# Kernel optimization log

Measured on AMD Instinct MI355X. Metric: run time of the kernel, lower is better.

Reference implementation:

```python
import jax, jax.numpy as jnp
import numpy as np

B, T, N, F_, H, C, E = 8, 16, 1024, 128, 8, 32, 32768
D = H * C  # 256 = hidden_channels * num_heads
NEG_SLOPE = 0.2


def setup_inputs() -> dict:
    key = jax.random.key(0)
    ks = jax.random.split(key, 16)
    p = lambda k, shape: (jax.random.normal(k, shape, jnp.float32) * 0.05)
    inp = {
        "x": jax.random.normal(ks[0], (B, T, N, F_), jnp.float32),
        "edge_index": jax.random.randint(ks[1], (2, E), 0, N, jnp.int64),
        "edge_weight": jax.random.uniform(ks[2], (E,), jnp.float32),
        # GAT layer 1
        "W1": p(ks[3], (F_, D)), "att_src1": p(ks[4], (H, C)),
        "att_dst1": p(ks[5], (H, C)), "b1": jnp.zeros((D,), jnp.float32),
        # GAT layer 2
        "W2": p(ks[6], (D, D)), "att_src2": p(ks[7], (H, C)),
        "att_dst2": p(ks[8], (H, C)), "b2": jnp.zeros((D,), jnp.float32),
        # LSTM (torch gate order: i, f, g, o)
        "lstm_Wih": p(ks[9], (4 * D, D)), "lstm_Whh": p(ks[10], (4 * D, D)),
        "lstm_bih": jnp.zeros((4 * D,), jnp.float32),
        "lstm_bhh": jnp.zeros((4 * D,), jnp.float32),
        # edge predictors
        "Wp": p(ks[11], (1, D)), "bp": jnp.zeros((1,), jnp.float32),
        "Wc": p(ks[12], (1, D)), "bc": jnp.zeros((1,), jnp.float32),
    }
    return inp


def _gat_layer(x2d, src, dst, W, a_src, a_dst, b):
    # x2d: [N, Fin]; src/dst: [Et] (self-loops already appended)
    h = (x2d @ W).reshape(N, H, C)              # [N, H, C]
    es = jnp.sum(h * a_src, axis=-1)            # [N, H]
    ed = jnp.sum(h * a_dst, axis=-1)            # [N, H]
    e = jax.nn.leaky_relu(es[src] + ed[dst], NEG_SLOPE)  # [Et, H]
    m = jax.ops.segment_max(e, dst, num_segments=N)      # [N, H]
    m = jnp.where(jnp.isfinite(m), m, 0.0)
    pnum = jnp.exp(e - m[dst])                  # [Et, H]
    denom = jax.ops.segment_sum(pnum, dst, num_segments=N)
    alpha = pnum / (denom[dst] + 1e-16)         # segment softmax over incoming edges
    out = jax.ops.segment_sum(alpha[:, :, None] * h[src], dst, num_segments=N)
    return out.reshape(N, D) + b                # concat heads + bias


def _forward(x, edge_index, edge_weight, W1, att_src1, att_dst1, b1,
             W2, att_src2, att_dst2, b2, lstm_Wih, lstm_Whh, lstm_bih,
             lstm_bhh, Wp, bp, Wc, bc):
    # GATConv ignores edge_weight when edge_dim is None (lin_edge is None).
    sl = jnp.arange(N, dtype=edge_index.dtype)
    src = jnp.concatenate([edge_index[0], sl])  # add_self_loops=True
    dst = jnp.concatenate([edge_index[1], sl])

    def per_graph(xi):  # xi: [N, F_]
        hh = jax.nn.relu(_gat_layer(xi, src, dst, W1, att_src1, att_dst1, b1))
        hh = jax.nn.relu(_gat_layer(hh, src, dst, W2, att_src2, att_dst2, b2))
        return hh  # [N, D]

    # stack timesteps then batches == reshape to [B*T, N, F_]
    hall = jax.vmap(per_graph)(x.reshape(B * T, N, F_))  # [B*T, N, D]

    # LSTM over the node dimension (batch_first=True, batch=B*T, seq=N)
    def step(carry, xt):
        hprev, cprev = carry
        z = xt @ lstm_Wih.T + hprev @ lstm_Whh.T + lstm_bih + lstm_bhh
        i, f, g, o = jnp.split(z, 4, axis=-1)
        c = jax.nn.sigmoid(f) * cprev + jax.nn.sigmoid(i) * jnp.tanh(g)
        hcur = jax.nn.sigmoid(o) * jnp.tanh(c)
        return (hcur, hcur * 0 + c)[0:1] * 0 or ((hcur, c), hcur)

    def step2(carry, xt):
        hprev, cprev = carry
        z = xt @ lstm_Wih.T + hprev @ lstm_Whh.T + lstm_bih + lstm_bhh
        i, f, g, o = jnp.split(z, 4, axis=-1)
        c = jax.nn.sigmoid(f) * cprev + jax.nn.sigmoid(i) * jnp.tanh(g)
        hcur = jax.nn.sigmoid(o) * jnp.tanh(c)
        return (hcur, c), hcur

    init = (jnp.zeros((B * T, D), hall.dtype), jnp.zeros((B * T, D), hall.dtype))
    _, hs = jax.lax.scan(step2, init, jnp.swapaxes(hall, 0, 1))  # [N, B*T, D]
    out = jnp.swapaxes(hs, 0, 1)      # [B*T, N, D]

    xsel = out[::T]                   # [B, N, D]
    xflat = xsel.reshape(B * N, D)
    xe = xflat[edge_index[0]] * xflat[edge_index[1]]  # [E, D]
    edge_weights_pred = xe @ Wp.T + bp                # [E, 1]
    logits = (xe @ Wc.T + bc).squeeze(-1)             # [E]
    return edge_weights_pred, logits


def reference(x, edge_index, edge_weight, W1, att_src1, att_dst1, b1,
              W2, att_src2, att_dst2, b2, lstm_Wih, lstm_Whh, lstm_bih,
              lstm_bhh, Wp, bp, Wc, bc):
    return _forward(x, edge_index, edge_weight, W1, att_src1, att_dst1, b1,
                    W2, att_src2, att_dst2, b2, lstm_Wih, lstm_Whh, lstm_bih,
                    lstm_bhh, Wp, bp, Wc, bc)
```

## Files before the change

kernel.cpp:

```cpp
#include <hip/hip_runtime.h>
#include <math.h>

#define NN 1024
#define FF 128
#define DD 256
#define HH 8
#define CC 32
#define EE 32768
#define NEDGE (EE + NN)

typedef unsigned int u32x2 __attribute__((ext_vector_type(2)));

__device__ __forceinline__ float sigf(float x) { return 1.0f / (1.0f + expf(-x)); }
__device__ __forceinline__ float fsig(float x) { return 1.0f / (1.0f + __expf(-x)); }
__device__ __forceinline__ float ftanh(float x) { return 2.0f / (1.0f + __expf(-2.0f * x)) - 1.0f; }

__device__ __forceinline__ void store_l2_u64(unsigned long long* p, unsigned long long v) {
  asm volatile("global_store_dwordx2 %0, %1, off sc0" :: "v"(p), "v"(v) : "memory");
}
__device__ __forceinline__ u32x2 load_l2_u64(const unsigned long long* p) {
  u32x2 r;
  asm volatile("global_load_dwordx2 %0, %1, off sc0\n\ts_waitcnt vmcnt(0)"
               : "=v"(r) : "v"(p) : "memory");
  return r;
}

__device__ __forceinline__ void barrier_lds() {
  asm volatile("s_waitcnt lgkmcnt(0)" ::: "memory");
  __builtin_amdgcn_sched_barrier(0);
  __builtin_amdgcn_s_barrier();
}

__global__ void k_count(const int* __restrict__ ei, int* __restrict__ count) {
  int k = blockIdx.x * blockDim.x + threadIdx.x;
  if (k >= NEDGE) return;
  int d = (k < EE) ? ei[EE + k] : (k - EE);
  atomicAdd(&count[d], 1);
}

__global__ void k_scan(const int* __restrict__ count, int* __restrict__ rowptr, int* __restrict__ cursor) {
  __shared__ int buf[NN];
  int t = threadIdx.x;
  int c = count[t];
  buf[t] = c;
  __syncthreads();
  for (int off = 1; off < NN; off <<= 1) {
    int add = (t >= off) ? buf[t - off] : 0;
    __syncthreads();
    buf[t] += add;
    __syncthreads();
  }
  int inc = buf[t];
  rowptr[t] = inc - c;
  cursor[t] = inc - c;
  if (t == NN - 1) rowptr[NN] = inc;
}

__global__ void k_scatter(const int* __restrict__ ei, int* __restrict__ cursor, int* __restrict__ csrc) {
  int k = blockIdx.x * blockDim.x + threadIdx.x;
  if (k >= NEDGE) return;
  int s, d;
  if (k < EE) { s = ei[k]; d = ei[EE + k]; }
  else        { s = k - EE; d = k - EE; }
  int pos = atomicAdd(&cursor[d], 1);
  csrc[pos] = s;
}

template<bool BT, bool ADDB>
__global__ __launch_bounds__(256) void k_gemm(const float* __restrict__ A, const float* __restrict__ B,
    const float* __restrict__ bias1, const float* __restrict__ bias2, float* __restrict__ C,
    int M, int N, int K) {
  __shared__ float At[64][17];
  __shared__ float Bt[16][65];
  const int tid = threadIdx.x;
  const int m0 = blockIdx.x * 64, n0 = blockIdx.y * 64;
  const int tx = tid & 15, ty = tid >> 4;
  float acc[4][4] = {{0.f, 0.f, 0.f, 0.f}};
  for (int k0 = 0; k0 < K; k0 += 16) {
    {
      int rr = tid >> 2, kl = (tid & 3) * 4;
      float4 a = *(const float4*)(A + (m0 + rr) * K + k0 + kl);
      At[rr][kl] = a.x; At[rr][kl + 1] = a.y; At[rr][kl + 2] = a.z; At[rr][kl + 3] = a.w;
    }
    if (BT) {
      int nn = tid >> 2, kl = (tid & 3) * 4;
      float4 b = *(const float4*)(B + (n0 + nn) * K + k0 + kl);
      Bt[kl][nn] = b.x; Bt[kl + 1][nn] = b.y; Bt[kl + 2][nn] = b.z; Bt[kl + 3][nn] = b.w;
    } else {
      int kk = tid >> 4, nn = (tid & 15) * 4;
      float4 b = *(const float4*)(B + (k0 + kk) * N + n0 + nn);
      Bt[kk][nn] = b.x; Bt[kk][nn + 1] = b.y; Bt[kk][nn + 2] = b.z; Bt[kk][nn + 3] = b.w;
    }
    __syncthreads();
    #pragma unroll
    for (int kk = 0; kk < 16; ++kk) {
      float av[4], bv[4];
      #pragma unroll
      for (int i = 0; i < 4; ++i) av[i] = At[ty * 4 + i][kk];
      #pragma unroll
      for (int jj = 0; jj < 4; ++jj) bv[jj] = Bt[kk][tx * 4 + jj];
      #pragma unroll
      for (int i = 0; i < 4; ++i)
        #pragma unroll
        for (int jj = 0; jj < 4; ++jj)
          acc[i][jj] = fmaf(av[i], bv[jj], acc[i][jj]);
    }
    __syncthreads();
  }
  #pragma unroll
  for (int i = 0; i < 4; ++i) {
    #pragma unroll
    for (int jj = 0; jj < 4; ++jj) {
      int n = n0 + tx * 4 + jj;
      float v = acc[i][jj];
      if (ADDB) v += bias1[n] + bias2[n];
      C[(m0 + ty * 4 + i) * N + n] = v;
    }
  }
}

__global__ __launch_bounds__(256) void k_att(const float* __restrict__ h, const float* __restrict__ asrc,
    const float* __restrict__ adst, float* __restrict__ es, float* __restrict__ ed) {
  int n = blockIdx.x;
  int hd = threadIdx.x >> 5, c = threadIdx.x & 31;
  float hv = h[n * DD + hd * CC + c];
  float e1 = hv * asrc[hd * CC + c];
  float e2 = hv * adst[hd * CC + c];
  #pragma unroll
  for (int msk = 1; msk < 32; msk <<= 1) { e1 += __shfl_xor(e1, msk); e2 += __shfl_xor(e2, msk); }
  if (c == 0) { es[n * HH + hd] = e1; ed[n * HH + hd] = e2; }
}

__global__ __launch_bounds__(256) void k_agg(const float* __restrict__ h, const float* __restrict__ es,
    const float* __restrict__ ed, const float* __restrict__ bias, const int* __restrict__ rowptr,
    const int* __restrict__ csrc, float* __restrict__ out) {
  int w = blockIdx.x * 4 + (threadIdx.x >> 6);
  int lane = threadIdx.x & 63;
  int n = w >> 3, hd = w & 7;
  int lo = rowptr[n], hi = rowptr[n + 1];
  float edn = ed[n * HH + hd];
  float m = -1e30f;
  for (int k = lo + lane; k < hi; k += 64) {
    int s = csrc[k];
    float e = es[s * HH + hd] + edn;
    e = (e > 0.f) ? e : 0.2f * e;
    m = fmaxf(m, e);
  }
  #pragma unroll
  for (int msk = 1; msk < 64; msk <<= 1) m = fmaxf(m, __shfl_xor(m, msk));
  float den = 0.f;
  for (int k = lo + lane; k < hi; k += 64) {
    int s = csrc[k];
    float e = es[s * HH + hd] + edn;
    e = (e > 0.f) ? e : 0.2f * e;
    den += expf(e - m);
  }
  #pragma unroll
  for (int msk = 1; msk < 64; msk <<= 1) den += __shfl_xor(den, msk);
  float inv = 1.0f / (den + 1e-16f);
  int c = lane & 31, halfsel = lane >> 5;
  float acc = 0.f;
  for (int k = lo + halfsel; k < hi; k += 2) {
    int s = csrc[k];
    float e = es[s * HH + hd] + edn;
    e = (e > 0.f) ? e : 0.2f * e;
    float al = expf(e - m) * inv;
    acc += al * h[s * DD + hd * CC + c];
  }
  acc += __shfl_down(acc, 32);
  if (lane < 32) {
    float v = acc + bias[hd * CC + c];
    out[n * DD + hd * CC + c] = fmaxf(v, 0.f);
  }
}

__global__ __launch_bounds__(512, 1) void k_lstm(const float* __restrict__ xW,
    const float* __restrict__ Whh, unsigned long long* __restrict__ fastw,
    unsigned long long* __restrict__ sloww, float* __restrict__ hs) {
  const int bid = blockIdx.x;
  const int coh = bid & 7;
  const int j = bid >> 3;
  unsigned long long* fw = fastw + coh * 2 * DD;
  unsigned long long* sw = sloww + coh * 2 * DD;
  const int t = threadIdx.x;
  const int r = t >> 2, qt = t & 3;
  const int g = r >> 5, kl = r & 31;
  const int grow = g * 256 + j * 32 + kl;
  __shared__ float hlds[DD];
  __shared__ float zlds[128];

  float wa[64];
  {
    const float4* W4 = (const float4*)(Whh + grow * DD + qt * 64);
    #pragma unroll
    for (int q = 0; q < 16; ++q) {
      const int qp = (q + 4 * qt) & 15;
      float4 tmp = W4[qp];
      asm volatile("v_accvgpr_write_b32 %0, %1" : "=a"(wa[4 * q + 0]) : "v"(tmp.x));
      asm volatile("v_accvgpr_write_b32 %0, %1" : "=a"(wa[4 * q + 1]) : "v"(tmp.y));
      asm volatile("v_accvgpr_write_b32 %0, %1" : "=a"(wa[4 * q + 2]) : "v"(tmp.z));
      asm volatile("v_accvgpr_write_b32 %0, %1" : "=a"(wa[4 * q + 3]) : "v"(tmp.w));
    }
  }
  if (t < DD) hlds[t] = 0.f;
  float creg = 0.f;
  float xwv = (qt == 0) ? xW[grow] : 0.f;
  int ftries = 64, lateMiss = 0;
  int bud = 1 << 20;
  __syncthreads();

  for (int s = 0; s < NN; ++s) {
    const float4* h4 = (const float4*)hlds + qt * 16;
    float ac4[4] = {0.f, 0.f, 0.f, 0.f};
    #pragma unroll
    for (int q = 0; q < 16; ++q) {
      const int qp = (q + 4 * qt) & 15;
      float4 hv = h4[qp];
      float w0, w1, w2, w3;
      asm volatile("v_accvgpr_read_b32 %0, %1" : "=v"(w0) : "a"(wa[4 * q + 0]));
      asm volatile("v_accvgpr_read_b32 %0, %1" : "=v"(w1) : "a"(wa[4 * q + 1]));
      asm volatile("v_accvgpr_read_b32 %0, %1" : "=v"(w2) : "a"(wa[4 * q + 2]));
      asm volatile("v_accvgpr_read_b32 %0, %1" : "=v"(w3) : "a"(wa[4 * q + 3]));
      ac4[q & 3] = fmaf(w0, hv.x, ac4[q & 3]);
      ac4[q & 3] = fmaf(w1, hv.y, ac4[q & 3]);
      ac4[q & 3] = fmaf(w2, hv.z, ac4[q & 3]);
      ac4[q & 3] = fmaf(w3, hv.w, ac4[q & 3]);
    }
    float acc = (ac4[0] + ac4[1]) + (ac4[2] + ac4[3]);
    acc += __shfl_xor(acc, 1);
    acc += __shfl_xor(acc, 2);
    if (qt == 0) zlds[r] = acc + xwv;
    barrier_lds();

    const int par = (s + 1) & 1;
    const unsigned int tag = (unsigned int)(s + 1);
    float xw_next = (qt == 0 && s + 1 < NN) ? xW[(s + 1) * 1024 + grow] : 0.f;

    if (t < 32) {
      float iv = zlds[t], fv = zlds[32 + t], gv = zlds[64 + t], ov = zlds[96 + t];
      creg = fsig(fv) * creg + fsig(iv) * ftanh(gv);
      float hn = fsig(ov) * ftanh(creg);
      int col = j * 32 + t;
      hlds[col] = hn;
      unsigned long long pk = ((unsigned long long)__float_as_uint(hn) << 32) | tag;
      store_l2_u64(&fw[par * DD + col], pk);
      __hip_atomic_store(&sw[par * DD + col], pk, __ATOMIC_RELAXED, __HIP_MEMORY_SCOPE_AGENT);
      hs[s * DD + col] = hn;
    } else if (t >= 64 && t < 288) {
      int pi = t - 64;
      int peer = j + 1 + (pi >> 5); if (peer >= 8) peer -= 8;
      int col = peer * 32 + (pi & 31);
      int idx = par * DD + col;
      u32x2 v; bool got = false;
      for (int tr = 0; tr < ftries; ++tr) {
        v = load_l2_u64(&fw[idx]);
        if (v.x == tag) { got = true; break; }
      }
      if (!got) {
        if (s >= 4) ++lateMiss;
        if (lateMiss >= 8 && ftries > 2) ftries = 2;
        unsigned long long a;
        for (;;) {
          a = __hip_atomic_load(&sw[idx], __ATOMIC_RELAXED, __HIP_MEMORY_SCOPE_AGENT);
          if ((unsigned int)(a & 0xffffffffULL) == tag) break;
          if (--bud <= 0) break;
          __builtin_amdgcn_s_sleep(1);
        }
        v.y = (unsigned int)(a >> 32);
      }
      hlds[col] = __uint_as_float(v.y);
    }
    barrier_lds();
    xwv = xw_next;
  }
}

__global__ __launch_bounds__(256) void k_edges(const float* __restrict__ hs, const int* __restrict__ ei,
    const float* __restrict__ Wp, const float* __restrict__ bp,
    const float* __restrict__ Wc, const float* __restrict__ bc, float* __restrict__ out) {
  int widx = threadIdx.x >> 6, lane = threadIdx.x & 63;
  int k = blockIdx.x * 4 + widx;
  int sIdx = ei[k], dIdx = ei[EE + k];
  float4 u = ((const float4*)(hs + sIdx * DD))[lane];
  float4 v = ((const float4*)(hs + dIdx * DD))[lane];
  float4 wp = ((const float4*)Wp)[lane];
  float4 wc = ((const float4*)Wc)[lane];
  float x0 = u.x * v.x, x1 = u.y * v.y, x2 = u.z * v.z, x3 = u.w * v.w;
  float ap = x0 * wp.x + x1 * wp.y + x2 * wp.z + x3 * wp.w;
  float ac = x0 * wc.x + x1 * wc.y + x2 * wc.z + x3 * wc.w;
  #pragma unroll
  for (int msk = 1; msk < 64; msk <<= 1) { ap += __shfl_xor(ap, msk); ac += __shfl_xor(ac, msk); }
  if (lane == 0) { out[k] = ap + bp[0]; out[EE + k] = ac + bc[0]; }
}

extern "C" void kernel_launch(void* const* d_in, const int* in_sizes, int n_in,
                              void* d_out, int out_size, void* d_ws, size_t ws_size,
                              hipStream_t stream) {
  const float* x       = (const float*)d_in[0];
  const int* ei        = (const int*)d_in[1];
  const float* W1      = (const float*)d_in[3];
  const float* as1     = (const float*)d_in[4];
  const float* ad1     = (const float*)d_in[5];
  const float* b1      = (const float*)d_in[6];
  const float* W2      = (const float*)d_in[7];
  const float* as2     = (const float*)d_in[8];
  const float* ad2     = (const float*)d_in[9];
  const float* b2      = (const float*)d_in[10];
  const float* Wih     = (const float*)d_in[11];
  const float* Whh     = (const float*)d_in[12];
  const float* bih     = (const float*)d_in[13];
  const float* bhh     = (const float*)d_in[14];
  const float* Wp      = (const float*)d_in[15];
  const float* bp      = (const float*)d_in[16];
  const float* Wc      = (const float*)d_in[17];
  const float* bc      = (const float*)d_in[18];
  float* out = (float*)d_out;

  char* ws = (char*)d_ws;
  int* counts                = (int*)(ws + 0);
  unsigned long long* fastw  = (unsigned long long*)(ws + 4096);
  unsigned long long* sloww  = (unsigned long long*)(ws + 36864);
  int* rowptr                = (int*)(ws + 69632);
  int* cursor                = (int*)(ws + 77824);
  int* csrc                  = (int*)(ws + 81920);
  float* es                  = (float*)(ws + 221184);
  float* ed                  = (float*)(ws + 253952);
  float* buf0                = (float*)(ws + 286720);
  float* buf1                = (float*)(ws + 1335296);
  float* xW                  = (float*)(ws + 2383872);
  float* hsall               = (float*)(ws + 6578176);

  hipMemsetAsync(ws, 0, 69632, stream);

  k_count  <<<(NEDGE + 255) / 256, 256, 0, stream>>>(ei, counts);
  k_scan   <<<1, 1024, 0, stream>>>(counts, rowptr, cursor);
  k_scatter<<<(NEDGE + 255) / 256, 256, 0, stream>>>(ei, cursor, csrc);

  k_gemm<false, false><<<dim3(16, 4), 256, 0, stream>>>(x, W1, nullptr, nullptr, buf0, NN, DD, FF);
  k_att<<<NN, 256, 0, stream>>>(buf0, as1, ad1, es, ed);
  k_agg<<<NN * HH / 4, 256, 0, stream>>>(buf0, es, ed, b1, rowptr, csrc, buf1);

  k_gemm<false, false><<<dim3(16, 4), 256, 0, stream>>>(buf1, W2, nullptr, nullptr, buf0, NN, DD, DD);
  k_att<<<NN, 256, 0, stream>>>(buf0, as2, ad2, es, ed);
  k_agg<<<NN * HH / 4, 256, 0, stream>>>(buf0, es, ed, b2, rowptr, csrc, buf1);

  k_gemm<true, true><<<dim3(16, 16), 256, 0, stream>>>(buf1, Wih, bih, bhh, xW, NN, 1024, DD);

  k_lstm<<<64, 512, 0, stream>>>(xW, Whh, fastw, sloww, hsall);

  k_edges<<<EE / 4, 256, 0, stream>>>(hsall, ei, Wp, bp, Wc, bc, out);
}
```

Measured before the change: 1.892 ms.

## Drop replicated LSTM cohorts and L2 fast path, use single agent-scope handoff

The recurrent LSTM kernel previously ran 8 redundant cohorts of 8 blocks. Each cohort exchanged hidden-state slices through a fast non-coherent L2 polling path, with an agent-scope atomic fallback that sleeps between polls. The new code launches one cohort of 8 blocks that exchange state only through relaxed agent-scope atomic loads and stores, with a tight spin and no sleep. This cuts redundant work, memset size and the polling logic. The cost is that blocks no longer share an L2 (blockIdx&7 no longer groups them), so each step's handoff likely has to cross XCDs and pay higher latency.

```diff
diff --git a/kernel.cpp b/kernel.cpp
--- a/kernel.cpp
+++ b/kernel.cpp
@@ -9,21 +9,9 @@
 #define EE 32768
 #define NEDGE (EE + NN)
 
-typedef unsigned int u32x2 __attribute__((ext_vector_type(2)));
-
 __device__ __forceinline__ float sigf(float x) { return 1.0f / (1.0f + expf(-x)); }
 __device__ __forceinline__ float fsig(float x) { return 1.0f / (1.0f + __expf(-x)); }
 __device__ __forceinline__ float ftanh(float x) { return 2.0f / (1.0f + __expf(-2.0f * x)) - 1.0f; }
-
-__device__ __forceinline__ void store_l2_u64(unsigned long long* p, unsigned long long v) {
-  asm volatile("global_store_dwordx2 %0, %1, off sc0" :: "v"(p), "v"(v) : "memory");
-}
-__device__ __forceinline__ u32x2 load_l2_u64(const unsigned long long* p) {
-  u32x2 r;
-  asm volatile("global_load_dwordx2 %0, %1, off sc0\n\ts_waitcnt vmcnt(0)"
-               : "=v"(r) : "v"(p) : "memory");
-  return r;
-}
 
 __device__ __forceinline__ void barrier_lds() {
   asm volatile("s_waitcnt lgkmcnt(0)" ::: "memory");
@@ -175,13 +163,9 @@
 }
 
 __global__ __launch_bounds__(512, 1) void k_lstm(const float* __restrict__ xW,
-    const float* __restrict__ Whh, unsigned long long* __restrict__ fastw,
-    unsigned long long* __restrict__ sloww, float* __restrict__ hs) {
-  const int bid = blockIdx.x;
-  const int coh = bid & 7;
-  const int j = bid >> 3;
-  unsigned long long* fw = fastw + coh * 2 * DD;
-  unsigned long long* sw = sloww + coh * 2 * DD;
+    const float* __restrict__ Whh, unsigned long long* __restrict__ sw,
+    float* __restrict__ hs) {
+  const int j = blockIdx.x;
   const int t = threadIdx.x;
   const int r = t >> 2, qt = t & 3;
   const int g = r >> 5, kl = r & 31;
@@ -205,8 +189,7 @@
   if (t < DD) hlds[t] = 0.f;
   float creg = 0.f;
   float xwv = (qt == 0) ? xW[grow] : 0.f;
-  int ftries = 64, lateMiss = 0;
-  int bud = 1 << 20;
+  int bud = 1 << 22;
   __syncthreads();
 
   for (int s = 0; s < NN; ++s) {
@@ -243,7 +226,6 @@
       int col = j * 32 + t;
       hlds[col] = hn;
       unsigned long long pk = ((unsigned long long)__float_as_uint(hn) << 32) | tag;
-      store_l2_u64(&fw[par * DD + col], pk);
       __hip_atomic_store(&sw[par * DD + col], pk, __ATOMIC_RELAXED, __HIP_MEMORY_SCOPE_AGENT);
       hs[s * DD + col] = hn;
     } else if (t >= 64 && t < 288) {
@@ -251,24 +233,13 @@
       int peer = j + 1 + (pi >> 5); if (peer >= 8) peer -= 8;
       int col = peer * 32 + (pi & 31);
       int idx = par * DD + col;
-      u32x2 v; bool got = false;
-      for (int tr = 0; tr < ftries; ++tr) {
-        v = load_l2_u64(&fw[idx]);
-        if (v.x == tag) { got = true; break; }
+      unsigned long long a;
+      for (;;) {
+        a = __hip_atomic_load(&sw[idx], __ATOMIC_RELAXED, __HIP_MEMORY_SCOPE_AGENT);
+        if ((unsigned int)(a & 0xffffffffULL) == tag) break;
+        if (--bud <= 0) break;
       }
-      if (!got) {
-        if (s >= 4) ++lateMiss;
-        if (lateMiss >= 8 && ftries > 2) ftries = 2;
-        unsigned long long a;
-        for (;;) {
-          a = __hip_atomic_load(&sw[idx], __ATOMIC_RELAXED, __HIP_MEMORY_SCOPE_AGENT);
-          if ((unsigned int)(a & 0xffffffffULL) == tag) break;
-          if (--bud <= 0) break;
-          __builtin_amdgcn_s_sleep(1);
-        }
-        v.y = (unsigned int)(a >> 32);
-      }
-      hlds[col] = __uint_as_float(v.y);
+      hlds[col] = __uint_as_float((unsigned int)(a >> 32));
     }
     barrier_lds();
     xwv = xw_next;
@@ -318,19 +289,18 @@
 
   char* ws = (char*)d_ws;
   int* counts                = (int*)(ws + 0);
-  unsigned long long* fastw  = (unsigned long long*)(ws + 4096);
-  unsigned long long* sloww  = (unsigned long long*)(ws + 36864);
-  int* rowptr                = (int*)(ws + 69632);
-  int* cursor                = (int*)(ws + 77824);
-  int* csrc                  = (int*)(ws + 81920);
-  float* es                  = (float*)(ws + 221184);
-  float* ed                  = (float*)(ws + 253952);
-  float* buf0                = (float*)(ws + 286720);
-  float* buf1                = (float*)(ws + 1335296);
-  float* xW                  = (float*)(ws + 2383872);
-  float* hsall               = (float*)(ws + 6578176);
-
-  hipMemsetAsync(ws, 0, 69632, stream);
+  unsigned long long* sloww  = (unsigned long long*)(ws + 4096);
+  int* rowptr                = (int*)(ws + 8192);
+  int* cursor                = (int*)(ws + 16384);
+  int* csrc                  = (int*)(ws + 20480);
+  float* es                  = (float*)(ws + 163840);
+  float* ed                  = (float*)(ws + 196608);
+  float* buf0                = (float*)(ws + 229376);
+  float* buf1                = (float*)(ws + 1277952);
+  float* xW                  = (float*)(ws + 2326528);
+  float* hsall               = (float*)(ws + 6520832);
+
+  hipMemsetAsync(ws, 0, 8192, stream);
 
   k_count  <<<(NEDGE + 255) / 256, 256, 0, stream>>>(ei, counts);
   k_scan   <<<1, 1024, 0, stream>>>(counts, rowptr, cursor);
@@ -346,7 +316,7 @@
 
   k_gemm<true, true><<<dim3(16, 16), 256, 0, stream>>>(buf1, Wih, bih, bhh, xW, NN, 1024, DD);
 
-  k_lstm<<<64, 512, 0, stream>>>(xW, Whh, fastw, sloww, hsall);
+  k_lstm<<<8, 512, 0, stream>>>(xW, Whh, sloww, hsall);
 
   k_edges<<<EE / 4, 256, 0, stream>>>(hsall, ei, Wp, bp, Wc, bc, out);
 }
```

After: 1.978 ms. +4.5%, slower.
